# Kernel optimization log

Hardware: AMD Instinct MI355X
Metric: run time of the kernel (lower is better)

## Reference

```python
import jax, jax.numpy as jnp
import numpy as np

E = 512
H = 8
D = E // H  # head_dim = 64
SCALE = D ** -0.5
NEG_INF = float('-inf')


def layer_norm(x, g, b, eps=1e-5):
    mu = jnp.mean(x, axis=-1, keepdims=True)
    var = jnp.var(x, axis=-1, keepdims=True)
    return (x - mu) * jax.lax.rsqrt(var + eps) * g + b


def setup_inputs() -> dict:
    key = jax.random.key(0)
    ks = jax.random.split(key, 16)
    B, Q, K = 4, 2048, 2048
    inp = {
        'query': jax.random.normal(ks[0], (B, Q, E), jnp.float32),
        'key_value': jax.random.normal(ks[1], (B, K, E), jnp.float32),
        'kv_mask': jax.random.randint(ks[2], (B, K), 0, 2) > 0,
        'sparse_mask': jax.random.randint(ks[3], (B, Q, K), 0, 2) > 0,
        'ln_q_g': jnp.ones((E,), jnp.float32),
        'ln_q_b': jnp.zeros((E,), jnp.float32),
        'ln_kv_g': jnp.ones((E,), jnp.float32),
        'ln_kv_b': jnp.zeros((E,), jnp.float32),
        # Linear weights stored as (in, out): y = x @ W + b
        'Wq': jax.random.normal(ks[4], (E, E), jnp.float32) * (E ** -0.5),
        'bq': jnp.zeros((E,), jnp.float32),
        'Wk': jax.random.normal(ks[5], (E, E), jnp.float32) * (E ** -0.5),
        'bk': jnp.zeros((E,), jnp.float32),
        'Wv': jax.random.normal(ks[6], (E, E), jnp.float32) * (E ** -0.5),
        'bv': jnp.zeros((E,), jnp.float32),
        'Wo': jax.random.normal(ks[7], (E, E), jnp.float32) * (E ** -0.5),
        'bo': jnp.zeros((E,), jnp.float32),
    }
    return inp


def reference(query, key_value, kv_mask, sparse_mask,
              ln_q_g, ln_q_b, ln_kv_g, ln_kv_b,
              Wq, bq, Wk, bk, Wv, bv, Wo, bo):
    B, Qn, _ = query.shape
    Kn = key_value.shape[1]
    qn = layer_norm(query, ln_q_g, ln_q_b)
    kvn = layer_norm(key_value, ln_kv_g, ln_kv_b)
    q = (qn @ Wq + bq).reshape(B, Qn, H, D)
    k = (kvn @ Wk + bk).reshape(B, Kn, H, D)
    v = (kvn @ Wv + bv).reshape(B, Kn, H, D)
    # scores: [B, H, Q, K]
    scores = jnp.einsum('bqhd,bkhd->bhqk', q, k) * SCALE
    mask = kv_mask[:, None, None, :] & sparse_mask[:, None, :, :]
    scores = jnp.where(mask, scores, NEG_INF)
    attn = jax.nn.softmax(scores, axis=-1)
    # nan_to_num(0): rows with no valid key -> all-zero weights
    valid_row = jnp.any(mask, axis=-1, keepdims=True)
    attn = jnp.where(valid_row, attn, 0.0)
    out = jnp.einsum('bhqk,bkhd->bqhd', attn, v).reshape(B, Qn, E)
    return out @ Wo + bo
```

## Files before the change

### kernel.cpp

```cpp
#include <hip/hip_runtime.h>
#include <hip/hip_bf16.h>
#include <math.h>

typedef unsigned short ushort_t;
typedef __attribute__((ext_vector_type(8))) __bf16 bf16x8;
typedef __attribute__((ext_vector_type(4))) float f32x4;
typedef __attribute__((ext_vector_type(4))) unsigned int u32x4;

#define E_DIM 512
#define HEADS 8
#define HD 64
#define SEQ 2048
#define NROWS 8192
#define NEGF (-1e30f)
#define QSCALE 0.18033688011112042f

static __device__ __forceinline__ unsigned short f2b(float f) {
  unsigned int x;
  __builtin_memcpy(&x, &f, 4);
  x += 0x7fffu + ((x >> 16) & 1u);
  return (unsigned short)(x >> 16);
}

static __device__ __forceinline__ int swz(int row, int col) {
  return row * 64 + ((((col >> 3) ^ (row & 7)) & 7) << 3) + (col & 7);
}

static __device__ __forceinline__ void gl2lds16(const ushort_t* g, ushort_t* s) {
#if __has_builtin(__builtin_amdgcn_global_load_lds)
  __builtin_amdgcn_global_load_lds(
      (const __attribute__((address_space(1))) unsigned int*)(uintptr_t)g,
      (__attribute__((address_space(3))) unsigned int*)(uintptr_t)s,
      16, 0, 0);
#else
  int l = threadIdx.x & 63;
  *(u32x4*)(s + l * 8) = *(const u32x4*)g;
#endif
}

__launch_bounds__(256)
__global__ void prep_kernel(const float* __restrict__ Wq, const float* __restrict__ Wk,
                            const float* __restrict__ Wv, const float* __restrict__ Wo,
                            ushort_t* __restrict__ WT,
                            const int* __restrict__ kvm, const int* __restrict__ sp,
                            unsigned long long* __restrict__ bits,
                            const float* __restrict__ xq, const float* __restrict__ xkv,
                            const float* __restrict__ gq, const float* __restrict__ bq,
                            const float* __restrict__ gkv, const float* __restrict__ bkv,
                            ushort_t* __restrict__ yq, ushort_t* __restrict__ ykv) {
  int blk = blockIdx.x;
  int t = threadIdx.x;
  if (blk < 1024) {
    int z = blk >> 8, rem = blk & 255;
    const float* in = (z == 0) ? Wq : (z == 1) ? Wk : (z == 2) ? Wv : Wo;
    ushort_t* o = WT + (size_t)z * E_DIM * E_DIM;
    __shared__ float tile[32 * 33];
    int tx = t & 31, ty = t >> 5;
    int n0 = (rem & 15) * 32, k0 = (rem >> 4) * 32;
#pragma unroll
    for (int i = 0; i < 4; ++i) {
      int k = ty + i * 8;
      tile[k * 33 + tx] = in[(k0 + k) * E_DIM + n0 + tx];
    }
    __syncthreads();
#pragma unroll
    for (int i = 0; i < 4; ++i) {
      int n = ty + i * 8;
      o[(n0 + n) * E_DIM + k0 + tx] = f2b(tile[tx * 33 + n]);
    }
  } else if (blk < 3072) {
    int w = t >> 6, l = t & 63;
    int row = (blk - 1024) * 4 + w;
    int b = row >> 11;
    const int* sprow = sp + ((size_t)row << 11);
    const int* kvrow = kvm + (b << 11);
    unsigned long long* out = bits + ((size_t)row << 5);
#pragma unroll 4
    for (int it = 0; it < 32; ++it) {
      int k = it * 64 + l;
      unsigned long long m = __ballot(sprow[k] != 0 && kvrow[k] != 0);
      if (l == 0) out[it] = m;
    }
  } else {
    int idx = blk - 3072;
    int which = idx >> 11;
    const float* x = which ? xkv : xq;
    const float* g = which ? gkv : gq;
    const float* bb = which ? bkv : bq;
    ushort_t* y = which ? ykv : yq;
    int w = t >> 6, l = t & 63;
    int row = (idx & 2047) * 4 + w;
    f32x4 x0 = *(const f32x4*)&x[row * E_DIM + l * 8];
    f32x4 x1 = *(const f32x4*)&x[row * E_DIM + l * 8 + 4];
    float xf[8], s = 0.f, ss = 0.f;
#pragma unroll
    for (int j = 0; j < 8; ++j) {
      xf[j] = (j < 4) ? x0[j] : x1[j - 4];
      s += xf[j];
      ss += xf[j] * xf[j];
    }
#pragma unroll
    for (int off = 32; off > 0; off >>= 1) {
      s += __shfl_xor(s, off);
      ss += __shfl_xor(ss, off);
    }
    float mu = s * (1.f / 512.f);
    float var = fmaxf(ss * (1.f / 512.f) - mu * mu, 0.f);
    float rs = rsqrtf(var + 1e-5f);
    f32x4 g0 = *(const f32x4*)&g[l * 8];
    f32x4 g1 = *(const f32x4*)&g[l * 8 + 4];
    f32x4 b0 = *(const f32x4*)&bb[l * 8];
    f32x4 b1 = *(const f32x4*)&bb[l * 8 + 4];
#pragma unroll
    for (int j = 0; j < 8; ++j) {
      float gv = (j < 4) ? g0[j] : g1[j - 4];
      float bv = (j < 4) ? b0[j] : b1[j - 4];
      y[row * E_DIM + l * 8 + j] = f2b((xf[j] - mu) * rs * gv + bv);
    }
  }
}

template <int MODE>
static __device__ __forceinline__ void gemm_core128(ushort_t* lA, ushort_t* lB,
                                                    const ushort_t* __restrict__ A,
                                                    const ushort_t* __restrict__ WT,
                                                    const float* __restrict__ bias,
                                                    void* Cv, float scale, int m0, int n0) {
  int t = threadIdx.x, w = t >> 6, l = t & 63;
  int quad = l >> 4, l15 = l & 15;
  int wm_ = w >> 1, wn_ = w & 1;
  int csrc = ((l & 7) ^ (l >> 3)) * 8;
  int rln = l >> 3;

  f32x4 acc[4][4] = {};
  for (int kk = 0; kk < E_DIM; kk += 64) {
    __syncthreads();
#pragma unroll
    for (int i = 0; i < 4; ++i) {
      int r0 = i * 32 + w * 8;
      gl2lds16(&A[(size_t)(m0 + r0 + rln) * E_DIM + kk + csrc], &lA[r0 * 64]);
      gl2lds16(&WT[(size_t)(n0 + r0 + rln) * E_DIM + kk + csrc], &lB[r0 * 64]);
    }
    __syncthreads();
#pragma unroll
    for (int ks = 0; ks < 2; ++ks) {
      bf16x8 af[4], bf[4];
#pragma unroll
      for (int mt = 0; mt < 4; ++mt)
        af[mt] = *(const bf16x8*)&lA[swz(wm_ * 64 + mt * 16 + l15, ks * 32 + quad * 8)];
#pragma unroll
      for (int nt = 0; nt < 4; ++nt)
        bf[nt] = *(const bf16x8*)&lB[swz(wn_ * 64 + nt * 16 + l15, ks * 32 + quad * 8)];
#pragma unroll
      for (int mt = 0; mt < 4; ++mt)
#pragma unroll
        for (int nt = 0; nt < 4; ++nt)
          acc[mt][nt] = __builtin_amdgcn_mfma_f32_16x16x32_bf16(af[mt], bf[nt], acc[mt][nt], 0, 0, 0);
    }
  }

#pragma unroll
  for (int nt = 0; nt < 4; ++nt) {
    int col = n0 + wn_ * 64 + nt * 16 + l15;
    float bv = bias[col];
    if constexpr (MODE == 2) {
      int h = col >> 6, d = col & 63;
#pragma unroll
      for (int mt = 0; mt < 4; ++mt) {
        int row = m0 + wm_ * 64 + mt * 16 + quad * 4;
        int b = row >> 11, k = row & 2047;
        union { ushort_t u[4]; uint2 v; } pk;
#pragma unroll
        for (int r = 0; r < 4; ++r) pk.u[r] = f2b(acc[mt][nt][r] + bv);
        *(uint2*)&((ushort_t*)Cv)[((((size_t)(b * HEADS + h)) * HD + d) << 11) + k] = pk.v;
      }
    } else {
#pragma unroll
      for (int mt = 0; mt < 4; ++mt) {
#pragma unroll
        for (int r = 0; r < 4; ++r) {
          int rowm = m0 + wm_ * 64 + mt * 16 + quad * 4 + r;
          float val = (acc[mt][nt][r] + bv) * scale;
          if constexpr (MODE == 0)
            ((ushort_t*)Cv)[rowm * E_DIM + col] = f2b(val);
          else
            ((float*)Cv)[rowm * E_DIM + col] = val;
        }
      }
    }
  }
}

__launch_bounds__(256)
__global__ void gemm128_bf16(const ushort_t* __restrict__ A, const ushort_t* __restrict__ WT,
                             const float* __restrict__ bias, ushort_t* __restrict__ C, float scale) {
  __shared__ ushort_t lA[128 * 64];
  __shared__ ushort_t lB[128 * 64];
  gemm_core128<0>(lA, lB, A, WT, bias, C, scale, blockIdx.x * 128, blockIdx.y * 128);
}

__launch_bounds__(256)
__global__ void gemm128_f32(const ushort_t* __restrict__ A, const ushort_t* __restrict__ WT,
                            const float* __restrict__ bias, float* __restrict__ C) {
  __shared__ ushort_t lA[128 * 64];
  __shared__ ushort_t lB[128 * 64];
  gemm_core128<1>(lA, lB, A, WT, bias, C, 1.f, blockIdx.x * 128, blockIdx.y * 128);
}

__launch_bounds__(256)
__global__ void proj2_kernel(const ushort_t* __restrict__ qn, const ushort_t* __restrict__ WTq,
                             const float* __restrict__ bq, ushort_t* __restrict__ qp,
                             const ushort_t* __restrict__ kvn, const ushort_t* __restrict__ WTv,
                             const float* __restrict__ bv, ushort_t* __restrict__ Vt) {
  __shared__ ushort_t lA[128 * 64];
  __shared__ ushort_t lB[128 * 64];
  int m0 = blockIdx.x * 128, n0 = blockIdx.y * 128;
  if (blockIdx.z == 0) gemm_core128<0>(lA, lB, qn, WTq, bq, qp, QSCALE, m0, n0);
  else                 gemm_core128<2>(lA, lB, kvn, WTv, bv, Vt, 1.f, m0, n0);
}

__launch_bounds__(256)
__global__ void attn_kernel(const ushort_t* __restrict__ Qp, const ushort_t* __restrict__ Kp,
                            const ushort_t* __restrict__ Vt,
                            const unsigned long long* __restrict__ bits,
                            ushort_t* __restrict__ ctx) {
  __shared__ ushort_t sQ[64 * 64];
  __shared__ ushort_t sK[64 * 64];
  __shared__ ushort_t sVt[64 * 64];
  __shared__ ushort_t sP[64 * 64];
  int t = threadIdx.x, w = t >> 6, l = t & 63;
  int quad = l >> 4, l15 = l & 15;
  int q0 = blockIdx.x * 64;
  int h = blockIdx.y;
  int b = blockIdx.z;
  int bh = b * HEADS + h;
  int myq = w * 16 + l15;
  int csrc = ((l & 7) ^ (l >> 3)) * 8;
  int rln = l >> 3;

#pragma unroll
  for (int it = 0; it < 2; ++it) {
    int r0 = it * 32 + w * 8;
    gl2lds16(&Qp[(size_t)(b * SEQ + q0 + r0 + rln) * E_DIM + h * HD + csrc], &sQ[r0 * 64]);
  }

  const unsigned long long* mrow = bits + ((size_t)(b * SEQ + q0 + myq) << 5);
  float lsum = 0.f;
  f32x4 o[4] = {};

  for (int kt = 0; kt < 32; ++kt) {
    int k0 = kt * 64;
    __syncthreads();
#pragma unroll
    for (int it = 0; it < 2; ++it) {
      int r0 = it * 32 + w * 8;
      gl2lds16(&Kp[(size_t)(b * SEQ + k0 + r0 + rln) * E_DIM + h * HD + csrc], &sK[r0 * 64]);
      gl2lds16(&Vt[((size_t)bh * HD + r0 + rln) * SEQ + k0 + csrc], &sVt[r0 * 64]);
    }
    __syncthreads();

    f32x4 s[4] = {};
#pragma unroll
    for (int ks = 0; ks < 2; ++ks) {
      bf16x8 qf = *(const bf16x8*)&sQ[swz(myq, ks * 32 + quad * 8)];
#pragma unroll
      for (int nt = 0; nt < 4; ++nt) {
        bf16x8 kf = *(const bf16x8*)&sK[swz(nt * 16 + l15, ks * 32 + quad * 8)];
        s[nt] = __builtin_amdgcn_mfma_f32_16x16x32_bf16(kf, qf, s[nt], 0, 0, 0);
      }
    }

    unsigned long long wmask = mrow[kt];
    unsigned sx = ((unsigned)wmask) >> (quad * 4);
    unsigned sy = ((unsigned)(wmask >> 32)) >> (quad * 4);
#pragma unroll
    for (int nt = 0; nt < 4; ++nt) {
      unsigned wsel = (nt & 2) ? sy : sx;
      int sh = (nt & 1) ? 16 : 0;
      union { ushort_t u[4]; uint2 v; } pk;
#pragma unroll
      for (int r = 0; r < 4; ++r) {
        float smv = ((wsel >> (sh + r)) & 1u) ? s[nt][r] : NEGF;
        float pv = exp2f(smv);
        pk.u[r] = (unsigned short)(__float_as_uint(pv) >> 16);
        lsum += pv;
      }
      *(uint2*)&sP[swz(myq, nt * 16 + quad * 4)] = pk.v;
    }

#pragma unroll
    for (int ks = 0; ks < 2; ++ks) {
      bf16x8 pf = *(const bf16x8*)&sP[swz(myq, ks * 32 + quad * 8)];
#pragma unroll
      for (int mt = 0; mt < 4; ++mt) {
        bf16x8 vf = *(const bf16x8*)&sVt[swz(mt * 16 + l15, ks * 32 + quad * 8)];
        o[mt] = __builtin_amdgcn_mfma_f32_16x16x32_bf16(vf, pf, o[mt], 0, 0, 0);
      }
    }
  }

  lsum += __shfl_xor(lsum, 16);
  lsum += __shfl_xor(lsum, 32);
  float inv = (lsum > 0.f) ? 1.f / lsum : 0.f;
  size_t base = (size_t)(b * SEQ + q0 + myq) * E_DIM + h * HD;
#pragma unroll
  for (int mt = 0; mt < 4; ++mt) {
    union { ushort_t u[4]; uint2 v; } ov;
#pragma unroll
    for (int r = 0; r < 4; ++r) ov.u[r] = f2b(o[mt][r] * inv);
    *(uint2*)&ctx[base + mt * 16 + quad * 4] = ov.v;
  }
}

extern "C" void kernel_launch(void* const* d_in, const int* in_sizes, int n_in,
                              void* d_out, int out_size, void* d_ws, size_t ws_size,
                              hipStream_t stream) {
  const float* query     = (const float*)d_in[0];
  const float* key_value = (const float*)d_in[1];
  const int*   kv_mask   = (const int*)d_in[2];
  const int*   sp_mask   = (const int*)d_in[3];
  const float* ln_q_g  = (const float*)d_in[4];
  const float* ln_q_b  = (const float*)d_in[5];
  const float* ln_kv_g = (const float*)d_in[6];
  const float* ln_kv_b = (const float*)d_in[7];
  const float* Wq = (const float*)d_in[8];
  const float* bq = (const float*)d_in[9];
  const float* Wk = (const float*)d_in[10];
  const float* bk = (const float*)d_in[11];
  const float* Wv = (const float*)d_in[12];
  const float* bv = (const float*)d_in[13];
  const float* Wo = (const float*)d_in[14];
  const float* bo = (const float*)d_in[15];

  const size_t NB = (size_t)NROWS * E_DIM;
  char* ws = (char*)d_ws;
  ushort_t* bufA = (ushort_t*)ws;
  ushort_t* bufB = bufA + NB;
  ushort_t* WT   = bufB + NB;
  ushort_t* WTq = WT;
  ushort_t* WTk = WTq + E_DIM * E_DIM;
  ushort_t* WTv = WTk + E_DIM * E_DIM;
  ushort_t* WTo = WTv + E_DIM * E_DIM;
  unsigned long long* bits = (unsigned long long*)(WTo + E_DIM * E_DIM);

  ushort_t* dlo = (ushort_t*)d_out;
  ushort_t* dhi = dlo + NB;

  prep_kernel<<<7168, 256, 0, stream>>>(Wq, Wk, Wv, Wo, WT, kv_mask, sp_mask, bits,
                                        query, key_value, ln_q_g, ln_q_b, ln_kv_g, ln_kv_b,
                                        dlo, bufA);

  proj2_kernel<<<dim3(64, 4, 2), 256, 0, stream>>>(dlo, WTq, bq, dhi,
                                                   bufA, WTv, bv, bufB);

  gemm128_bf16<<<dim3(64, 4), 256, 0, stream>>>(bufA, WTk, bk, dlo, 1.f);

  attn_kernel<<<dim3(32, HEADS, 4), 256, 0, stream>>>(dhi, dlo, bufB, bits, bufA);

  gemm128_f32<<<dim3(64, 4), 256, 0, stream>>>(bufA, WTo, bo, (float*)d_out);
}
```

Baseline: 289.5 us.

## Switch attention to 32x32x16 MFMA with 128-query tiles and register-held Q

The attention kernel now processes 128 queries per block, 32 per wave, using 32x32x16 bf16 MFMA instructions instead of 16x16x32. Q fragments are loaded into registers once at the first key tile and reused for all key tiles. Each K/V tile loaded into LDS is therefore shared by twice as many queries, halving K/V global traffic and LDS reads per query. The cost is more accumulator registers, more LDS for Q and P, and half as many blocks in the grid, which may lower occupancy.

```diff
diff --git a/kernel.cpp b/kernel.cpp
--- a/kernel.cpp
+++ b/kernel.cpp
@@ -5,6 +5,7 @@
 typedef unsigned short ushort_t;
 typedef __attribute__((ext_vector_type(8))) __bf16 bf16x8;
 typedef __attribute__((ext_vector_type(4))) float f32x4;
+typedef __attribute__((ext_vector_type(16))) float f32x16;
 typedef __attribute__((ext_vector_type(4))) unsigned int u32x4;
 
 #define E_DIM 512
@@ -224,29 +225,30 @@
                             const ushort_t* __restrict__ Vt,
                             const unsigned long long* __restrict__ bits,
                             ushort_t* __restrict__ ctx) {
-  __shared__ ushort_t sQ[64 * 64];
+  __shared__ ushort_t sQ[128 * 64];
   __shared__ ushort_t sK[64 * 64];
   __shared__ ushort_t sVt[64 * 64];
-  __shared__ ushort_t sP[64 * 64];
+  __shared__ ushort_t sP[128 * 64];
   int t = threadIdx.x, w = t >> 6, l = t & 63;
-  int quad = l >> 4, l15 = l & 15;
-  int q0 = blockIdx.x * 64;
+  int l31 = l & 31, half = l >> 5;
+  int q0 = blockIdx.x * 128;
   int h = blockIdx.y;
   int b = blockIdx.z;
   int bh = b * HEADS + h;
-  int myq = w * 16 + l15;
+  int myq = w * 32 + l31;
   int csrc = ((l & 7) ^ (l >> 3)) * 8;
   int rln = l >> 3;
 
 #pragma unroll
-  for (int it = 0; it < 2; ++it) {
+  for (int it = 0; it < 4; ++it) {
     int r0 = it * 32 + w * 8;
     gl2lds16(&Qp[(size_t)(b * SEQ + q0 + r0 + rln) * E_DIM + h * HD + csrc], &sQ[r0 * 64]);
   }
 
   const unsigned long long* mrow = bits + ((size_t)(b * SEQ + q0 + myq) << 5);
   float lsum = 0.f;
-  f32x4 o[4] = {};
+  f32x16 o0 = {}, o1 = {};
+  bf16x8 qf[4];
 
   for (int kt = 0; kt < 32; ++kt) {
     int k0 = kt * 64;
@@ -258,57 +260,64 @@
       gl2lds16(&Vt[((size_t)bh * HD + r0 + rln) * SEQ + k0 + csrc], &sVt[r0 * 64]);
     }
     __syncthreads();
-
-    f32x4 s[4] = {};
-#pragma unroll
-    for (int ks = 0; ks < 2; ++ks) {
-      bf16x8 qf = *(const bf16x8*)&sQ[swz(myq, ks * 32 + quad * 8)];
-#pragma unroll
-      for (int nt = 0; nt < 4; ++nt) {
-        bf16x8 kf = *(const bf16x8*)&sK[swz(nt * 16 + l15, ks * 32 + quad * 8)];
-        s[nt] = __builtin_amdgcn_mfma_f32_16x16x32_bf16(kf, qf, s[nt], 0, 0, 0);
+    if (kt == 0) {
+#pragma unroll
+      for (int ds = 0; ds < 4; ++ds)
+        qf[ds] = *(const bf16x8*)&sQ[swz(myq, ds * 16 + 8 * half)];
+    }
+
+    f32x16 s0 = {}, s1 = {};
+#pragma unroll
+    for (int ds = 0; ds < 4; ++ds) {
+      bf16x8 kf0 = *(const bf16x8*)&sK[swz(l31, ds * 16 + 8 * half)];
+      bf16x8 kf1 = *(const bf16x8*)&sK[swz(32 + l31, ds * 16 + 8 * half)];
+      s0 = __builtin_amdgcn_mfma_f32_32x32x16_bf16(kf0, qf[ds], s0, 0, 0, 0);
+      s1 = __builtin_amdgcn_mfma_f32_32x32x16_bf16(kf1, qf[ds], s1, 0, 0, 0);
+    }
+
+    unsigned long long wmask = mrow[kt];
+#pragma unroll
+    for (int kt2 = 0; kt2 < 2; ++kt2) {
+      const f32x16& sv = kt2 ? s1 : s0;
+      unsigned h32 = ((unsigned)(wmask >> (32 * kt2))) >> (4 * half);
+#pragma unroll
+      for (int g = 0; g < 4; ++g) {
+        unsigned gb = h32 >> (8 * g);
+        union { ushort_t u[4]; uint2 v; } pk;
+#pragma unroll
+        for (int r = 0; r < 4; ++r) {
+          float smv = ((gb >> r) & 1u) ? sv[g * 4 + r] : NEGF;
+          float pv = exp2f(smv);
+          pk.u[r] = (unsigned short)(__float_as_uint(pv) >> 16);
+          lsum += pv;
+        }
+        *(uint2*)&sP[swz(myq, kt2 * 32 + g * 8 + 4 * half)] = pk.v;
       }
     }
 
-    unsigned long long wmask = mrow[kt];
-    unsigned sx = ((unsigned)wmask) >> (quad * 4);
-    unsigned sy = ((unsigned)(wmask >> 32)) >> (quad * 4);
-#pragma unroll
-    for (int nt = 0; nt < 4; ++nt) {
-      unsigned wsel = (nt & 2) ? sy : sx;
-      int sh = (nt & 1) ? 16 : 0;
-      union { ushort_t u[4]; uint2 v; } pk;
-#pragma unroll
-      for (int r = 0; r < 4; ++r) {
-        float smv = ((wsel >> (sh + r)) & 1u) ? s[nt][r] : NEGF;
-        float pv = exp2f(smv);
-        pk.u[r] = (unsigned short)(__float_as_uint(pv) >> 16);
-        lsum += pv;
-      }
-      *(uint2*)&sP[swz(myq, nt * 16 + quad * 4)] = pk.v;
-    }
-
-#pragma unroll
-    for (int ks = 0; ks < 2; ++ks) {
-      bf16x8 pf = *(const bf16x8*)&sP[swz(myq, ks * 32 + quad * 8)];
-#pragma unroll
-      for (int mt = 0; mt < 4; ++mt) {
-        bf16x8 vf = *(const bf16x8*)&sVt[swz(mt * 16 + l15, ks * 32 + quad * 8)];
-        o[mt] = __builtin_amdgcn_mfma_f32_16x16x32_bf16(vf, pf, o[mt], 0, 0, 0);
-      }
-    }
-  }
-
-  lsum += __shfl_xor(lsum, 16);
+#pragma unroll
+    for (int ksp = 0; ksp < 4; ++ksp) {
+      bf16x8 pf = *(const bf16x8*)&sP[swz(myq, ksp * 16 + 8 * half)];
+      bf16x8 vf0 = *(const bf16x8*)&sVt[swz(l31, ksp * 16 + 8 * half)];
+      bf16x8 vf1 = *(const bf16x8*)&sVt[swz(32 + l31, ksp * 16 + 8 * half)];
+      o0 = __builtin_amdgcn_mfma_f32_32x32x16_bf16(vf0, pf, o0, 0, 0, 0);
+      o1 = __builtin_amdgcn_mfma_f32_32x32x16_bf16(vf1, pf, o1, 0, 0, 0);
+    }
+  }
+
   lsum += __shfl_xor(lsum, 32);
   float inv = (lsum > 0.f) ? 1.f / lsum : 0.f;
   size_t base = (size_t)(b * SEQ + q0 + myq) * E_DIM + h * HD;
 #pragma unroll
-  for (int mt = 0; mt < 4; ++mt) {
-    union { ushort_t u[4]; uint2 v; } ov;
-#pragma unroll
-    for (int r = 0; r < 4; ++r) ov.u[r] = f2b(o[mt][r] * inv);
-    *(uint2*)&ctx[base + mt * 16 + quad * 4] = ov.v;
+  for (int dt = 0; dt < 2; ++dt) {
+    const f32x16& oo = dt ? o1 : o0;
+#pragma unroll
+    for (int g = 0; g < 4; ++g) {
+      union { ushort_t u[4]; uint2 v; } ov;
+#pragma unroll
+      for (int r = 0; r < 4; ++r) ov.u[r] = f2b(oo[g * 4 + r] * inv);
+      *(uint2*)&ctx[base + dt * 32 + g * 8 + 4 * half] = ov.v;
+    }
   }
 }
 
@@ -355,7 +364,7 @@
 
   gemm128_bf16<<<dim3(64, 4), 256, 0, stream>>>(bufA, WTk, bk, dlo, 1.f);
 
-  attn_kernel<<<dim3(32, HEADS, 4), 256, 0, stream>>>(dhi, dlo, bufB, bits, bufA);
+  attn_kernel<<<dim3(16, HEADS, 4), 256, 0, stream>>>(dhi, dlo, bufB, bits, bufA);
 
   gemm128_f32<<<dim3(64, 4), 256, 0, stream>>>(bufA, WTo, bo, (float*)d_out);
 }
```

Result: no change. 286.0 us (-1.2%).
